# Kernel tuning notes

Measured on AMD Instinct MI355X. Metric: run time of the kernel, lower is better.

Reference implementation:

```python
import jax, jax.numpy as jnp
import numpy as np

D = 256  # channel dim and CBP output dim


def setup_inputs() -> dict:
    key = jax.random.key(0)
    ks = jax.random.split(key, 14)
    B, C, H, W = 32, 256, 56, 56
    attr_num = 400
    inp = {}
    inp["entity_feature"] = jax.random.normal(ks[0], (B, C, H, W), jnp.float32)
    inp["attr_one_hot"] = jax.random.uniform(ks[1], (B, attr_num), jnp.float32)
    # textual_emb: Linear(attr_num, 256)
    inp["W_emb"] = jax.random.normal(ks[2], (D, attr_num), jnp.float32) * 0.02
    inp["b_emb"] = jnp.zeros((D,), jnp.float32)
    # conv: Conv2d(256,256,1)
    inp["conv_w"] = jax.random.normal(ks[3], (D, D), jnp.float32) * 0.02
    inp["conv_b"] = jnp.zeros((D,), jnp.float32)
    # mcb_conv1_attr: Conv2d(256,32,1)
    inp["conv1_w"] = jax.random.normal(ks[4], (32, D), jnp.float32) * 0.05
    inp["conv1_b"] = jnp.zeros((32,), jnp.float32)
    # mcb_conv2_attr: Conv2d(32,1,1)
    inp["conv2_w"] = jax.random.normal(ks[5], (1, 32), jnp.float32) * 0.1
    inp["conv2_b"] = jnp.zeros((1,), jnp.float32)
    # CompactBilinearPooling count-sketch tables (fixed random at init)
    inp["h1"] = jax.random.randint(ks[6], (D,), 0, D, jnp.int32)
    inp["h2"] = jax.random.randint(ks[7], (D,), 0, D, jnp.int32)
    inp["s1"] = (jax.random.randint(ks[8], (D,), 0, 2, jnp.int32) * 2 - 1).astype(jnp.float32)
    inp["s2"] = (jax.random.randint(ks[9], (D,), 0, 2, jnp.int32) * 2 - 1).astype(jnp.float32)
    return inp


def _sketch_matrix(h, s):
    # sparse count-sketch projection as dense [C_in, D] matrix: P[i, h[i]] = s[i]
    return jnp.zeros((D, D), jnp.float32).at[jnp.arange(D), h].add(s)


def reference(entity_feature, attr_one_hot, W_emb, b_emb, conv_w, conv_b,
              conv1_w, conv1_b, conv2_w, conv2_b, h1, h2, s1, s2):
    feature = jax.nn.relu(entity_feature)                      # [B,256,H,W]
    # textual embedding + spatially-constant 1x1 conv (identical math to
    # expanding then convolving, since the expanded tensor is constant over HxW)
    t = attr_one_hot @ W_emb.T + b_emb                         # [B,256]
    a = t @ conv_w.T + conv_b                                  # [B,256]

    # Compact Bilinear Pooling (count sketch -> FFT -> elementwise mul -> iFFT)
    P1 = _sketch_matrix(h1, s1)
    P2 = _sketch_matrix(h2, s2)
    sk1 = a @ P1                                               # [B,256], spatially constant
    sk2 = jnp.einsum('bchw,cd->bdhw', feature, P2)             # [B,256,H,W]
    fft1 = jnp.fft.rfft(sk1, n=D, axis=1)[:, :, None, None]    # [B,129,1,1]
    fft2 = jnp.fft.rfft(sk2, n=D, axis=1)                      # [B,129,H,W]
    mcb = jnp.fft.irfft(fft1 * fft2, n=D, axis=1)              # [B,256,H,W]

    # gating chain: conv1x1 -> relu -> conv1x1 -> sigmoid
    x = jax.nn.relu(jnp.einsum('bchw,oc->bohw', mcb, conv1_w) + conv1_b[None, :, None, None])
    attr_map = jax.nn.sigmoid(jnp.einsum('bchw,oc->bohw', x, conv2_w) + conv2_b[None, :, None, None])  # [B,1,H,W]
    attr_feature = attr_map * entity_feature                   # [B,256,H,W]
    return attr_map, attr_feature
```

## Files before the change

### kernel.cpp

```cpp
#include <hip/hip_runtime.h>

#define Dq   256
#define ATTR 400
#define HW   3136
#define NB   32

typedef __attribute__((ext_vector_type(8))) short bf16x8;
typedef __attribute__((ext_vector_type(4))) float f32x4;

__device__ __forceinline__ unsigned short f2bf(float f) {
  unsigned int x = __float_as_uint(f);
  return (unsigned short)((x + 0x7FFFu + ((x >> 16) & 1u)) >> 16);
}

__global__ __launch_bounds__(256) void k_sk1(
    const float* __restrict__ oh, const float* __restrict__ W_emb,
    const float* __restrict__ b_emb, const float* __restrict__ conv_w,
    const float* __restrict__ conv_b, const int* __restrict__ h1,
    const float* __restrict__ s1, float* __restrict__ sk1_out) {
  __shared__ float ohs[ATTR];
  __shared__ float ts[Dq];
  __shared__ float sk[Dq];
  const int b = blockIdx.x, tid = threadIdx.x;
  for (int j = tid; j < ATTR; j += 256) ohs[j] = oh[b * ATTR + j];
  sk[tid] = 0.f;
  __syncthreads();
  float acc = b_emb[tid];
  const float* wr = W_emb + tid * ATTR;
  for (int j = 0; j < ATTR; ++j) acc = fmaf(ohs[j], wr[j], acc);
  ts[tid] = acc;
  __syncthreads();
  float a = conv_b[tid];
  const float* cr = conv_w + tid * Dq;
  for (int k = 0; k < Dq; ++k) a = fmaf(ts[k], cr[k], a);
  atomicAdd(&sk[h1[tid]], a * s1[tid]);
  __syncthreads();
  sk1_out[b * Dq + tid] = sk[tid];
}

__global__ __launch_bounds__(256) void k_G(
    const float* __restrict__ sk1, const float* __restrict__ conv1_w,
    const int* __restrict__ h2, const float* __restrict__ s2,
    unsigned short* __restrict__ Abuf) {
  __shared__ float sks[Dq];
  __shared__ float w1[Dq];
  __shared__ float Tl[Dq];
  const int b = blockIdx.x >> 5, o = blockIdx.x & 31, c = threadIdx.x;
  sks[c] = sk1[b * Dq + c];
  w1[c]  = conv1_w[o * Dq + c];
  __syncthreads();
  float t = 0.f;
  for (int d = 0; d < Dq; ++d) t = fmaf(w1[d], sks[(d - c) & 255], t);
  Tl[c] = t;
  __syncthreads();
  const float g = s2[c] * Tl[h2[c]];
  const int frag = (o >> 4) * 8 + (c >> 5);
  const int lane = (o & 15) | (((c >> 3) & 3) << 4);
  Abuf[(((size_t)b * 16 + frag) * 64 + lane) * 8 + (c & 7)] = f2bf(g);
}

__global__ __launch_bounds__(256, 4) void k_fused(
    const float* __restrict__ ent,
    const unsigned short* __restrict__ Abuf,
    const float* __restrict__ c1b, const float* __restrict__ c2w,
    const float* __restrict__ c2b,
    float* __restrict__ out)
{
  __shared__ float sv[64];
  const int b = blockIdx.y, tid = threadIdx.x;
  const int w = tid >> 6, l = tid & 63;
  const int px0 = blockIdx.x * 64 + w * 16;

  bf16x8 A0[8], A1[8];
  const unsigned short* Ab = Abuf + ((size_t)b * 16 * 64 + l) * 8;
#pragma unroll
  for (int ks = 0; ks < 8; ++ks) {
    A0[ks] = *reinterpret_cast<const bf16x8*>(Ab + (size_t)(0 * 8 + ks) * 64 * 8);
    A1[ks] = *reinterpret_cast<const bf16x8*>(Ab + (size_t)(1 * 8 + ks) * 64 * 8);
  }

  f32x4 acc0 = {0.f, 0.f, 0.f, 0.f}, acc1 = {0.f, 0.f, 0.f, 0.f};
  const float* ep = ent + (size_t)b * Dq * HW + px0 + (l & 15);
  const int krow = (l >> 4) * 8;

#pragma unroll
  for (int ks = 0; ks < 8; ++ks) {
    float f[8];
#pragma unroll
    for (int j = 0; j < 8; ++j)
      f[j] = fmaxf(ep[(size_t)(ks * 32 + krow + j) * HW], 0.f);
    bf16x8 bv;
#pragma unroll
    for (int j = 0; j < 8; ++j) bv[j] = (short)f2bf(f[j]);
    acc0 = __builtin_amdgcn_mfma_f32_16x16x32_bf16(A0[ks], bv, acc0, 0, 0, 0);
    acc1 = __builtin_amdgcn_mfma_f32_16x16x32_bf16(A1[ks], bv, acc1, 0, 0, 0);
  }

  const float4 b1a = reinterpret_cast<const float4*>(c1b)[l >> 4];
  const float4 b1b = reinterpret_cast<const float4*>(c1b)[(l >> 4) + 4];
  const float4 w2a = reinterpret_cast<const float4*>(c2w)[l >> 4];
  const float4 w2b = reinterpret_cast<const float4*>(c2w)[(l >> 4) + 4];
  float z = 0.f;
  z = fmaf(w2a.x, fmaxf(acc0[0] + b1a.x, 0.f), z);
  z = fmaf(w2a.y, fmaxf(acc0[1] + b1a.y, 0.f), z);
  z = fmaf(w2a.z, fmaxf(acc0[2] + b1a.z, 0.f), z);
  z = fmaf(w2a.w, fmaxf(acc0[3] + b1a.w, 0.f), z);
  z = fmaf(w2b.x, fmaxf(acc1[0] + b1b.x, 0.f), z);
  z = fmaf(w2b.y, fmaxf(acc1[1] + b1b.y, 0.f), z);
  z = fmaf(w2b.z, fmaxf(acc1[2] + b1b.z, 0.f), z);
  z = fmaf(w2b.w, fmaxf(acc1[3] + b1b.w, 0.f), z);
  z += __shfl_xor(z, 16);
  z += __shfl_xor(z, 32);
  const float s = 1.f / (1.f + __expf(-(z + c2b[0])));
  if (l < 16) {
    out[(size_t)b * HW + px0 + l] = s;
    sv[w * 16 + l] = s;
  }
  __syncthreads();

  const float sval = sv[l];
  const size_t basep = (size_t)b * Dq * HW + (size_t)blockIdx.x * 64 + l + (size_t)w * HW;
  const float* ep2 = ent + basep;
  float* fp2 = out + (size_t)NB * HW + basep;
#pragma unroll 8
  for (int cc = 0; cc < 64; ++cc) {
    float v = ep2[(size_t)cc * 4 * HW];
    __builtin_nontemporal_store(sval * v, &fp2[(size_t)cc * 4 * HW]);
  }
}

extern "C" void kernel_launch(void* const* d_in, const int* in_sizes, int n_in,
                              void* d_out, int out_size, void* d_ws, size_t ws_size,
                              hipStream_t stream) {
  const float* ent    = (const float*)d_in[0];
  const float* oh     = (const float*)d_in[1];
  const float* W_emb  = (const float*)d_in[2];
  const float* b_emb  = (const float*)d_in[3];
  const float* conv_w = (const float*)d_in[4];
  const float* conv_b = (const float*)d_in[5];
  const float* c1w    = (const float*)d_in[6];
  const float* c1b    = (const float*)d_in[7];
  const float* c2w    = (const float*)d_in[8];
  const float* c2b    = (const float*)d_in[9];
  const int*   h1     = (const int*)d_in[10];
  const int*   h2     = (const int*)d_in[11];
  const float* s1     = (const float*)d_in[12];
  const float* s2     = (const float*)d_in[13];

  float* ws  = (float*)d_ws;
  float* sk1 = ws;
  unsigned short* Abuf = (unsigned short*)(ws + NB * Dq);

  hipLaunchKernelGGL(k_sk1, dim3(NB), dim3(256), 0, stream,
                     oh, W_emb, b_emb, conv_w, conv_b, h1, s1, sk1);
  hipLaunchKernelGGL(k_G, dim3(NB * 32), dim3(256), 0, stream,
                     sk1, c1w, h2, s2, Abuf);
  hipLaunchKernelGGL(k_fused, dim3(HW / 64, NB), dim3(256), 0, stream,
                     ent, Abuf, c1b, c2w, c2b, (float*)d_out);
}
```

Measured before the change: 80.65 us.

## Keep entity tile in registers and reuse it for gated output store

The fused kernel now loads each thread's 64 entity values once into registers, uses them for both the MFMA gating GEMM and the final gated output, and drops the second global read pass along with the shared-memory broadcast and block barrier. The A-fragments are loaded per k-step instead of all up front, which frees registers for the 64-float array. The cost is higher register pressure and therefore possibly lower occupancy. The output stores also become 16-wide strided segments per channel, which coalesce less well than the previous 64-wide rows.

```diff
diff --git a/kernel.cpp b/kernel.cpp
--- a/kernel.cpp
+++ b/kernel.cpp
@@ -66,34 +66,31 @@
     const float* __restrict__ c2b,
     float* __restrict__ out)
 {
-  __shared__ float sv[64];
   const int b = blockIdx.y, tid = threadIdx.x;
   const int w = tid >> 6, l = tid & 63;
   const int px0 = blockIdx.x * 64 + w * 16;
+  const int krow = (l >> 4) * 8;
 
-  bf16x8 A0[8], A1[8];
+  const float* ep = ent + (size_t)b * Dq * HW + px0 + (l & 15);
+
+  float e[64];
+#pragma unroll
+  for (int j = 0; j < 64; ++j) {
+    const int ch = (j >> 3) * 32 + krow + (j & 7);
+    e[j] = ep[(size_t)ch * HW];
+  }
+
   const unsigned short* Ab = Abuf + ((size_t)b * 16 * 64 + l) * 8;
+  f32x4 acc0 = {0.f, 0.f, 0.f, 0.f}, acc1 = {0.f, 0.f, 0.f, 0.f};
 #pragma unroll
   for (int ks = 0; ks < 8; ++ks) {
-    A0[ks] = *reinterpret_cast<const bf16x8*>(Ab + (size_t)(0 * 8 + ks) * 64 * 8);
-    A1[ks] = *reinterpret_cast<const bf16x8*>(Ab + (size_t)(1 * 8 + ks) * 64 * 8);
-  }
-
-  f32x4 acc0 = {0.f, 0.f, 0.f, 0.f}, acc1 = {0.f, 0.f, 0.f, 0.f};
-  const float* ep = ent + (size_t)b * Dq * HW + px0 + (l & 15);
-  const int krow = (l >> 4) * 8;
-
-#pragma unroll
-  for (int ks = 0; ks < 8; ++ks) {
-    float f[8];
-#pragma unroll
-    for (int j = 0; j < 8; ++j)
-      f[j] = fmaxf(ep[(size_t)(ks * 32 + krow + j) * HW], 0.f);
     bf16x8 bv;
 #pragma unroll
-    for (int j = 0; j < 8; ++j) bv[j] = (short)f2bf(f[j]);
-    acc0 = __builtin_amdgcn_mfma_f32_16x16x32_bf16(A0[ks], bv, acc0, 0, 0, 0);
-    acc1 = __builtin_amdgcn_mfma_f32_16x16x32_bf16(A1[ks], bv, acc1, 0, 0, 0);
+    for (int j = 0; j < 8; ++j) bv[j] = (short)f2bf(fmaxf(e[ks * 8 + j], 0.f));
+    bf16x8 a0 = *reinterpret_cast<const bf16x8*>(Ab + (size_t)(0 * 8 + ks) * 64 * 8);
+    bf16x8 a1 = *reinterpret_cast<const bf16x8*>(Ab + (size_t)(1 * 8 + ks) * 64 * 8);
+    acc0 = __builtin_amdgcn_mfma_f32_16x16x32_bf16(a0, bv, acc0, 0, 0, 0);
+    acc1 = __builtin_amdgcn_mfma_f32_16x16x32_bf16(a1, bv, acc1, 0, 0, 0);
   }
 
   const float4 b1a = reinterpret_cast<const float4*>(c1b)[l >> 4];
@@ -112,20 +109,14 @@
   z += __shfl_xor(z, 16);
   z += __shfl_xor(z, 32);
   const float s = 1.f / (1.f + __expf(-(z + c2b[0])));
-  if (l < 16) {
-    out[(size_t)b * HW + px0 + l] = s;
-    sv[w * 16 + l] = s;
-  }
-  __syncthreads();
 
-  const float sval = sv[l];
-  const size_t basep = (size_t)b * Dq * HW + (size_t)blockIdx.x * 64 + l + (size_t)w * HW;
-  const float* ep2 = ent + basep;
-  float* fp2 = out + (size_t)NB * HW + basep;
-#pragma unroll 8
-  for (int cc = 0; cc < 64; ++cc) {
-    float v = ep2[(size_t)cc * 4 * HW];
-    __builtin_nontemporal_store(sval * v, &fp2[(size_t)cc * 4 * HW]);
+  if (l < 16) out[(size_t)b * HW + px0 + l] = s;
+
+  float* fp = out + (size_t)NB * HW + (size_t)b * Dq * HW + px0 + (l & 15);
+#pragma unroll
+  for (int j = 0; j < 64; ++j) {
+    const int ch = (j >> 3) * 32 + krow + (j & 7);
+    __builtin_nontemporal_store(s * e[j], &fp[(size_t)ch * HW]);
   }
 }
 
```

Result: faster. 73.32 us (-9.1%).
